# Kernel tuning notes

Measured on AMD Instinct MI355X. Metric: run time of the kernel, lower is better.

## Reference

```python
import jax, jax.numpy as jnp
import numpy as np
from jax import lax

B, N, DIM, H, HD = 4, 8192, 256, 8, 32
INTERNAL = H * HD  # 256
SCALE = HD ** -0.5


def rotate_every_two(x):
    x1 = x[..., ::2]
    x2 = x[..., 1::2]
    return jnp.stack([-x2, x1], axis=-1).reshape(x.shape)


def theta_shift(x, sin, cos):
    # sin/cos: (N, HD) broadcast against (B, H, N, HD)
    return x * cos + rotate_every_two(x) * sin


def setup_inputs() -> dict:
    key = jax.random.key(0)
    ks = jax.random.split(key, 8)
    x = jax.random.normal(ks[0], (B, N, DIM), jnp.float32)
    sin = jax.random.uniform(ks[1], (N, HD), jnp.float32)
    cos = jax.random.uniform(ks[2], (N, HD), jnp.float32)
    W_qkvo = jax.random.normal(ks[3], (4 * INTERNAL, DIM), jnp.float32) * 0.02
    b_qkvo = jnp.zeros((4 * INTERNAL,), jnp.float32)
    W_lepe = jax.random.normal(ks[4], (INTERNAL, 1, 3), jnp.float32) * 0.1  # depthwise conv (O, I/g=1, K)
    b_lepe = jnp.zeros((INTERNAL,), jnp.float32)
    W_proj = jax.random.normal(ks[5], (DIM, INTERNAL), jnp.float32) * 0.02
    b_proj = jnp.zeros((DIM,), jnp.float32)
    return {"x": x, "sin": sin, "cos": cos, "W_qkvo": W_qkvo, "b_qkvo": b_qkvo,
            "W_lepe": W_lepe, "b_lepe": b_lepe, "W_proj": W_proj, "b_proj": b_proj}


def reference(x, sin, cos, W_qkvo, b_qkvo, W_lepe, b_lepe, W_proj, b_proj):
    # qkvo projection and chunk
    qkvo = x @ W_qkvo.T + b_qkvo  # (B, N, 4*INTERNAL)
    q, k, v, o = jnp.split(qkvo, 4, axis=-1)

    # depthwise conv LEPE branch on v: (B, C, N)
    v_t = jnp.transpose(v, (0, 2, 1))
    lepe = lax.conv_general_dilated(
        v_t, W_lepe, window_strides=(1,), padding=[(1, 1)],
        dimension_numbers=("NCH", "OIH", "NCH"), feature_group_count=INTERNAL)
    lepe_out = jnp.transpose(lepe + b_lepe[None, :, None], (0, 2, 1))  # (B, N, INTERNAL)

    # split heads: (B, H, N, HD)
    def heads(t):
        return jnp.transpose(t.reshape(B, N, H, HD), (0, 2, 1, 3))
    qh, kh, vh = heads(q), heads(k), heads(v)

    qh = jax.nn.elu(qh) + 1.0
    kh = jax.nn.elu(kh) + 1.0

    # z: (B, H, N, 1) against per-head k mean
    kmean = kh.mean(axis=2, keepdims=True)  # (B, H, 1, HD)
    z = jnp.einsum("bhnd,bhmd->bhnm", qh, kmean) * SCALE

    qs = theta_shift(qh, sin, cos)
    ks_ = theta_shift(kh, sin, cos)

    s = (SCALE / N) ** 0.5
    kv_state = jnp.einsum("bhnd,bhne->bhde", ks_ * s, vh * s)  # (B, H, HD, HD)
    attn_out = jnp.einsum("bhnd,bhde->bhne", qs, kv_state)     # (B, H, N, HD)

    v_mean = vh.mean(axis=2, keepdims=True)  # (B, H, 1, HD)
    res = attn_out * (1.0 + 1.0 / (z + 1e-6)) - z * v_mean

    res = jnp.transpose(res, (0, 2, 1, 3)).reshape(B, N, INTERNAL)
    res = res + lepe_out
    return (res * o) @ W_proj.T + b_proj
```

## Files before the change

### kernel.cpp

```cpp
#include <hip/hip_runtime.h>
#include <hip/hip_bf16.h>


typedef __bf16 bf16x8 __attribute__((ext_vector_type(8)));
typedef float  f32x4  __attribute__((ext_vector_type(4)));
typedef float  f32x2  __attribute__((ext_vector_type(2)));

#define NSEQ  8192
#define TOK   32768
#define SCALE_F 0.17677669529663687f
#define S2_F    2.1579674718339462e-05f

__device__ __forceinline__ bf16x8 ld8(const __bf16* p) { return *(const bf16x8*)p; }
__device__ __forceinline__ bf16x8 ld8(const float* p) {
  f32x4 a = *(const f32x4*)p;
  f32x4 b = *(const f32x4*)(p + 4);
  bf16x8 r;
  r[0]=(__bf16)a.x; r[1]=(__bf16)a.y; r[2]=(__bf16)a.z; r[3]=(__bf16)a.w;
  r[4]=(__bf16)b.x; r[5]=(__bf16)b.y; r[6]=(__bf16)b.z; r[7]=(__bf16)b.w;
  return r;
}

template<int EPI, typename TA, typename TB, typename TO>
__global__ __launch_bounds__(256)
void gemm_kernel(const TA* __restrict__ A, const TB* __restrict__ Bw,
                 const float* __restrict__ bias,
                 TO* __restrict__ o0, __bf16* __restrict__ o1,
                 __bf16* __restrict__ o2, __bf16* __restrict__ o3)
{
  constexpr int K = 256;
  __shared__ __align__(16) __bf16 As[128*32];
  __shared__ __align__(16) __bf16 Bs[128*32];
  const int tid  = threadIdx.x;
  const int lane = tid & 63;
  const int wid  = tid >> 6;
  const int wm = wid & 1, wn = wid >> 1;
  const long m0 = (long)blockIdx.x * 128;
  const int  n0 = blockIdx.y * 128;

  const TA* ag = A  + (m0 + (tid>>2))*K + (tid&3)*8;
  const TB* bg = Bw + (long)(n0 + (tid>>2))*K + (tid&3)*8;
  __bf16* asw = As + tid*8;
  __bf16* bsw = Bs + tid*8;

  f32x4 acc[4][4] = {};

  for (int k0 = 0; k0 < K; k0 += 32) {
    bf16x8 a0 = ld8(ag + k0);
    bf16x8 a1 = ld8(ag + 64*K + k0);
    bf16x8 b0 = ld8(bg + k0);
    bf16x8 b1 = ld8(bg + 64*K + k0);
    __syncthreads();
    *(bf16x8*)asw          = a0;
    *(bf16x8*)(asw + 2048) = a1;
    *(bf16x8*)bsw          = b0;
    *(bf16x8*)(bsw + 2048) = b1;
    __syncthreads();
    const int row = lane & 15;
    const int k8  = (lane >> 4) * 8;
    bf16x8 af[4], bfr[4];
#pragma unroll
    for (int i=0;i<4;i++) af[i]  = *(const bf16x8*)&As[(wm*64 + i*16 + row)*32 + k8];
#pragma unroll
    for (int j=0;j<4;j++) bfr[j] = *(const bf16x8*)&Bs[(wn*64 + j*16 + row)*32 + k8];
#pragma unroll
    for (int i=0;i<4;i++)
#pragma unroll
      for (int j=0;j<4;j++)
        acc[i][j] = __builtin_amdgcn_mfma_f32_16x16x32_bf16(af[i], bfr[j], acc[i][j], 0,0,0);
  }

#pragma unroll
  for (int i=0;i<4;i++) {
    const long t = m0 + wm*64 + i*16 + (lane>>4)*4;
#pragma unroll
    for (int j=0;j<4;j++) {
      const int cj = n0 + wn*64 + j*16 + (lane&15);
      const float bv = bias[cj];
      if (EPI == 1) {
        const int sec = cj >> 8;
        const int c   = cj & 255;
#pragma unroll
        for (int r=0;r<4;r++) {
          const long tt = t + r;
          float v = acc[i][j][r] + bv;
          if (sec < 2) v = (v > 0.f) ? (v + 1.f) : __expf(v);
          if (sec == 1) {
            const long bh = (tt >> 13)*8 + (c >> 5);
            o1[(bh*8192 + (tt & 8191))*32 + (c & 31)] = (__bf16)v;
          } else {
            __bf16* dst = (sec==0)?(__bf16*)o0:(sec==2)?o2:o3;
            dst[tt*256 + c] = (__bf16)v;
          }
        }
      } else {
#pragma unroll
        for (int r=0;r<4;r++)
          o0[(t+r)*256 + cj] = (TO)(acc[i][j][r] + bv);
      }
    }
  }
}

__global__ __launch_bounds__(256)
void reduce_kernel(const __bf16* __restrict__ kh_t, const __bf16* __restrict__ vv,
                   const float* __restrict__ sing, const float* __restrict__ cosg,
                   float* __restrict__ ksum, float* __restrict__ vsum,
                   float* __restrict__ kvT)
{
  __shared__ __align__(16) float ks_s[128*36];
  __shared__ __align__(16) float v_s[128*36];
  __shared__ float ksum_s[32], vsum_s[32];
  __shared__ float kvacc[1024];
  const int tid = threadIdx.x, lane = tid & 63, wid = tid >> 6;
  const int bh = blockIdx.x;
  const int b = bh >> 3, h = bh & 7;
  const int n0 = blockIdx.y * 512;
  const int seg = tid & 3;
  const int tksl = tid >> 2;

  if (tid < 32) { ksum_s[tid] = 0.f; vsum_s[tid] = 0.f; }
  for (int i = tid; i < 1024; i += 256) kvacc[i] = 0.f;

  float sk[8] = {}, sv[8] = {};
  f32x4 a0={},a1={},a2={},a3={};
  const int db = (lane>>3)*4, eb = (lane&7)*4;

  for (int sub = 0; sub < 4; sub++) {
    const int nbase = n0 + sub*128;
    __syncthreads();
#pragma unroll
    for (int i=0;i<2;i++) {
      const int tok = i*64 + tksl;
      const int n = nbase + tok;
      bf16x8 k8 = *(const bf16x8*)&kh_t[((long)bh*8192 + n)*32 + seg*8];
      bf16x8 w8 = *(const bf16x8*)&vv[((long)b*8192 + n)*256 + h*32 + seg*8];
      f32x4 cA = *(const f32x4*)&cosg[n*32 + seg*8];
      f32x4 cB = *(const f32x4*)&cosg[n*32 + seg*8 + 4];
      f32x4 sA = *(const f32x4*)&sing[n*32 + seg*8];
      f32x4 sB = *(const f32x4*)&sing[n*32 + seg*8 + 4];
      float kf[8], wf[8], cf[8], sf[8], ks[8];
#pragma unroll
      for (int j=0;j<8;j++) { kf[j]=(float)k8[j]; wf[j]=(float)w8[j]; }
      cf[0]=cA.x;cf[1]=cA.y;cf[2]=cA.z;cf[3]=cA.w;cf[4]=cB.x;cf[5]=cB.y;cf[6]=cB.z;cf[7]=cB.w;
      sf[0]=sA.x;sf[1]=sA.y;sf[2]=sA.z;sf[3]=sA.w;sf[4]=sB.x;sf[5]=sB.y;sf[6]=sB.z;sf[7]=sB.w;
#pragma unroll
      for (int j=0;j<8;j+=2) {
        ks[j]   = kf[j]*cf[j]     - kf[j+1]*sf[j];
        ks[j+1] = kf[j+1]*cf[j+1] + kf[j]*sf[j+1];
      }
      f32x4 q0 = {ks[0],ks[1],ks[2],ks[3]}, q1 = {ks[4],ks[5],ks[6],ks[7]};
      *(f32x4*)&ks_s[tok*36 + seg*8]     = q0;
      *(f32x4*)&ks_s[tok*36 + seg*8 + 4] = q1;
      f32x4 p0 = {wf[0],wf[1],wf[2],wf[3]}, p1 = {wf[4],wf[5],wf[6],wf[7]};
      *(f32x4*)&v_s[tok*36 + seg*8]     = p0;
      *(f32x4*)&v_s[tok*36 + seg*8 + 4] = p1;
#pragma unroll
      for (int j=0;j<8;j++) { sk[j] += kf[j]; sv[j] += wf[j]; }
    }
    __syncthreads();
    for (int t2 = 0; t2 < 32; t2++) {
      const int nl = wid*32 + t2;
      f32x4 kk = *(const f32x4*)&ks_s[nl*36 + db];
      f32x4 vp = *(const f32x4*)&v_s[nl*36 + eb];
      a0 += kk.x * vp;  a1 += kk.y * vp;  a2 += kk.z * vp;  a3 += kk.w * vp;
    }
  }

#pragma unroll
  for (int e=0;e<4;e++) {
    atomicAdd(&kvacc[(eb+e)*32 + db+0], a0[e]);
    atomicAdd(&kvacc[(eb+e)*32 + db+1], a1[e]);
    atomicAdd(&kvacc[(eb+e)*32 + db+2], a2[e]);
    atomicAdd(&kvacc[(eb+e)*32 + db+3], a3[e]);
  }
#pragma unroll
  for (int m = 4; m <= 32; m <<= 1) {
#pragma unroll
    for (int j=0;j<8;j++) { sk[j] += __shfl_xor(sk[j], m); sv[j] += __shfl_xor(sv[j], m); }
  }
  if (lane < 4) {
#pragma unroll
    for (int j=0;j<8;j++) {
      atomicAdd(&ksum_s[lane*8 + j], sk[j]);
      atomicAdd(&vsum_s[lane*8 + j], sv[j]);
    }
  }
  __syncthreads();
  float* dst = kvT + (long)bh*1024;
  for (int i = tid; i < 1024; i += 256) atomicAdd(&dst[i], kvacc[i]);
  if (tid < 32) { atomicAdd(&ksum[bh*32+tid], ksum_s[tid]);
                  atomicAdd(&vsum[bh*32+tid], vsum_s[tid]); }
}

__global__ __launch_bounds__(256)
void epi_kernel(const __bf16* __restrict__ qh, const __bf16* __restrict__ vv,
                const __bf16* __restrict__ oo,
                const float* __restrict__ sing, const float* __restrict__ cosg,
                const float* __restrict__ ksum, const float* __restrict__ vsum,
                const float* __restrict__ kvT,
                const float* __restrict__ Wl, const float* __restrict__ bl,
                __bf16* __restrict__ resf)
{
  __shared__ __align__(16) __bf16 qs_s[32*256];
  __shared__ __align__(16) __bf16 kv_s[8*32*32];
  __shared__ __align__(16) __bf16 lep_s[32*256];
  __shared__ float z_s[32*8];
  __shared__ float km_s[256], vm_s[256];
  const int tid = threadIdx.x, lane = tid & 63, wid = tid >> 6;
  const long t0 = (long)blockIdx.x * 32;
  const int b  = (int)(t0 >> 13);
  const int n0 = (int)(t0 & 8191);
  const int bh0 = b * 8;

  for (int i = tid; i < 8192; i += 256)
    kv_s[i] = (__bf16)(kvT[(long)bh0*1024 + i] * S2_F);
  km_s[tid] = ksum[bh0*32 + tid] * (1.f/8192.f);
  vm_s[tid] = vsum[bh0*32 + tid] * (1.f/8192.f);
  __syncthreads();

  for (int i=0;i<16;i++) {
    const int p  = i*256 + tid;
    const int t  = p >> 7;
    const int c2 = p & 127;
    const int h  = c2 >> 4;
    const int d0 = (c2 & 15) * 2;
    const long tg = t0 + t;
    const int n = n0 + t;
    const float q0 = (float)qh[tg*256 + h*32 + d0];
    const float q1 = (float)qh[tg*256 + h*32 + d0 + 1];
    f32x2 cp = *(const f32x2*)&cosg[n*32 + d0];
    f32x2 sp = *(const f32x2*)&sing[n*32 + d0];
    qs_s[t*256 + h*32 + d0]     = (__bf16)(q0*cp.x - q1*sp.x);
    qs_s[t*256 + h*32 + d0 + 1] = (__bf16)(q1*cp.y + q0*sp.y);
    float zp = q0*km_s[h*32+d0] + q1*km_s[h*32+d0+1];
    zp += __shfl_xor(zp, 1);
    zp += __shfl_xor(zp, 2);
    zp += __shfl_xor(zp, 4);
    zp += __shfl_xor(zp, 8);
    if ((lane & 15) == 0) z_s[t*8 + h] = zp * SCALE_F;
  }
  for (int i=0;i<32;i++) {
    const int f = i*256 + tid;
    const int t = f >> 8;
    const int c = f & 255;
    const long tg = t0 + t;
    const int n = n0 + t;
    const float vm1 = (n > 0)      ? (float)vv[(tg-1)*256 + c] : 0.f;
    const float v0  =                (float)vv[tg*256 + c];
    const float vp1 = (n < NSEQ-1) ? (float)vv[(tg+1)*256 + c] : 0.f;
    lep_s[f] = (__bf16)(vm1*Wl[c*3+0] + v0*Wl[c*3+1] + vp1*Wl[c*3+2] + bl[c]);
  }
  __syncthreads();

  const int e  = lane & 15;
  const int d8 = (lane >> 4) * 8;
  for (int hh=0; hh<2; hh++) {
    const int h = wid*2 + hh;
    bf16x8 bfr0 = *(const bf16x8*)&kv_s[h*1024 + e*32 + d8];
    bf16x8 bfr1 = *(const bf16x8*)&kv_s[h*1024 + (16+e)*32 + d8];
    for (int im=0; im<2; im++) {
      bf16x8 afr = *(const bf16x8*)&qs_s[(im*16 + e)*256 + h*32 + d8];
      for (int jn=0; jn<2; jn++) {
        f32x4 acc = {};
        acc = __builtin_amdgcn_mfma_f32_16x16x32_bf16(afr, jn ? bfr1 : bfr0, acc, 0,0,0);
        const int c = h*32 + jn*16 + e;
        const float vmn = vm_s[c];
#pragma unroll
        for (int r=0;r<4;r++) {
          const int t = im*16 + (lane>>4)*4 + r;
          const long tg = t0 + t;
          const float zv = z_s[t*8 + h];
          const float res = acc[r]*(1.f + 1.f/(zv + 1e-6f)) - zv*vmn
                            + (float)lep_s[t*256 + c];
          resf[tg*256 + c] = (__bf16)(res * (float)oo[tg*256 + c]);
        }
      }
    }
  }
}

extern "C" void kernel_launch(void* const* d_in, const int* in_sizes, int n_in,
                              void* d_out, int out_size, void* d_ws, size_t ws_size,
                              hipStream_t stream)
{
  const float* x    = (const float*)d_in[0];
  const float* sing = (const float*)d_in[1];
  const float* cosg = (const float*)d_in[2];
  const float* Wq   = (const float*)d_in[3];
  const float* bq   = (const float*)d_in[4];
  const float* Wl   = (const float*)d_in[5];
  const float* bl   = (const float*)d_in[6];
  const float* Wp   = (const float*)d_in[7];
  const float* bp   = (const float*)d_in[8];
  float* out = (float*)d_out;

  char* ws = (char*)d_ws;
  float*  ksum = (float*)(ws);
  float*  vsum = (float*)(ws + 4096);
  float*  kvT  = (float*)(ws + 8192);
  const size_t T0 = 256 * 1024;
  const size_t SZ = (size_t)TOK * 256 * sizeof(__bf16);
  __bf16* kh_t = (__bf16*)(ws + T0);
  __bf16* vv   = (__bf16*)(ws + T0 + SZ);
  __bf16* oo   = (__bf16*)(ws + T0 + 2*SZ);
  __bf16* qh   = (__bf16*)(ws + T0 + 3*SZ);
  __bf16* resf = kh_t;

  hipMemsetAsync(ws, 0, 8192 + 32*1024*4, stream);

  gemm_kernel<1,float,float,__bf16><<<dim3(256, 8), 256, 0, stream>>>(x, Wq, bq, qh, kh_t, vv, oo);
  reduce_kernel<<<dim3(32, 16), 256, 0, stream>>>(kh_t, vv, sing, cosg, ksum, vsum, kvT);
  epi_kernel<<<1024, 256, 0, stream>>>(qh, vv, oo, sing, cosg, ksum, vsum, kvT, Wl, bl, resf);
  gemm_kernel<2,__bf16,float,float><<<dim3(256, 2), 256, 0, stream>>>(resf, Wp, bp, out, nullptr, nullptr, nullptr);
}
```

Measured before the change: 225.2 us.

## Pre-convert GEMM inputs to bf16 and load tiles via global_load_lds

Adds conversion kernels that turn x and both weight matrices into bf16 buffers in workspace, so both GEMMs read only bf16. Tile staging then uses direct global-to-LDS loads instead of loading through registers and storing to shared memory. The aim is to shrink register traffic and conversion work inside the GEMM loop. In exchange it adds three launches and an extra full pass over x (read fp32, write bf16). The epilogue output buffer is moved to reuse the converted-x buffer.

Measured after the change: 213.3 us. -5.3%, faster.

```diff
diff --git a/kernel.cpp b/kernel.cpp
--- a/kernel.cpp
+++ b/kernel.cpp
@@ -11,8 +11,13 @@
 #define SCALE_F 0.17677669529663687f
 #define S2_F    2.1579674718339462e-05f
 
-__device__ __forceinline__ bf16x8 ld8(const __bf16* p) { return *(const bf16x8*)p; }
-__device__ __forceinline__ bf16x8 ld8(const float* p) {
+__device__ __forceinline__ void gld16(void* lds, const void* g) {
+  __builtin_amdgcn_global_load_lds((const __attribute__((address_space(1))) void*)g,
+                                   (__attribute__((address_space(3))) void*)lds,
+                                   16, 0, 0);
+}
+
+__device__ __forceinline__ bf16x8 cvt8(const float* p) {
   f32x4 a = *(const f32x4*)p;
   f32x4 b = *(const f32x4*)(p + 4);
   bf16x8 r;
@@ -21,9 +26,17 @@
   return r;
 }
 
-template<int EPI, typename TA, typename TB, typename TO>
 __global__ __launch_bounds__(256)
-void gemm_kernel(const TA* __restrict__ A, const TB* __restrict__ Bw,
+void cvt_kernel(const float* __restrict__ src, __bf16* __restrict__ dst, int n8)
+{
+  const int i = blockIdx.x*256 + threadIdx.x;
+  if (i >= n8) return;
+  *(bf16x8*)(dst + (long)i*8) = cvt8(src + (long)i*8);
+}
+
+template<int EPI, typename TO>
+__global__ __launch_bounds__(256)
+void gemm_kernel(const __bf16* __restrict__ A, const __bf16* __restrict__ Bw,
                  const float* __restrict__ bias,
                  TO* __restrict__ o0, __bf16* __restrict__ o1,
                  __bf16* __restrict__ o2, __bf16* __restrict__ o3)
@@ -38,23 +51,19 @@
   const long m0 = (long)blockIdx.x * 128;
   const int  n0 = blockIdx.y * 128;
 
-  const TA* ag = A  + (m0 + (tid>>2))*K + (tid&3)*8;
-  const TB* bg = Bw + (long)(n0 + (tid>>2))*K + (tid&3)*8;
+  const __bf16* ag = A  + (m0 + (tid>>2))*K + (tid&3)*8;
+  const __bf16* bg = Bw + (long)(n0 + (tid>>2))*K + (tid&3)*8;
   __bf16* asw = As + tid*8;
   __bf16* bsw = Bs + tid*8;
 
   f32x4 acc[4][4] = {};
 
   for (int k0 = 0; k0 < K; k0 += 32) {
-    bf16x8 a0 = ld8(ag + k0);
-    bf16x8 a1 = ld8(ag + 64*K + k0);
-    bf16x8 b0 = ld8(bg + k0);
-    bf16x8 b1 = ld8(bg + 64*K + k0);
     __syncthreads();
-    *(bf16x8*)asw          = a0;
-    *(bf16x8*)(asw + 2048) = a1;
-    *(bf16x8*)bsw          = b0;
-    *(bf16x8*)(bsw + 2048) = b1;
+    gld16(asw,        ag + k0);
+    gld16(asw + 2048, ag + 64*K + k0);
+    gld16(bsw,        bg + k0);
+    gld16(bsw + 2048, bg + 64*K + k0);
     __syncthreads();
     const int row = lane & 15;
     const int k8  = (lane >> 4) * 8;
@@ -305,12 +314,19 @@
   __bf16* vv   = (__bf16*)(ws + T0 + SZ);
   __bf16* oo   = (__bf16*)(ws + T0 + 2*SZ);
   __bf16* qh   = (__bf16*)(ws + T0 + 3*SZ);
-  __bf16* resf = kh_t;
+  __bf16* xbf  = (__bf16*)(ws + T0 + 4*SZ);
+  __bf16* Wqb  = (__bf16*)(ws + T0 + 5*SZ);
+  __bf16* Wpb  = (__bf16*)(ws + T0 + 5*SZ + 512*1024);
+  __bf16* resf = xbf;
 
   hipMemsetAsync(ws, 0, 8192 + 32*1024*4, stream);
 
-  gemm_kernel<1,float,float,__bf16><<<dim3(256, 8), 256, 0, stream>>>(x, Wq, bq, qh, kh_t, vv, oo);
+  cvt_kernel<<<4096, 256, 0, stream>>>(x,  xbf, TOK*256/8);
+  cvt_kernel<<<128,  256, 0, stream>>>(Wq, Wqb, 1024*256/8);
+  cvt_kernel<<<32,   256, 0, stream>>>(Wp, Wpb, 256*256/8);
+
+  gemm_kernel<1,__bf16><<<dim3(256, 8), 256, 0, stream>>>(xbf, Wqb, bq, qh, kh_t, vv, oo);
   reduce_kernel<<<dim3(32, 16), 256, 0, stream>>>(kh_t, vv, sing, cosg, ksum, vsum, kvT);
   epi_kernel<<<1024, 256, 0, stream>>>(qh, vv, oo, sing, cosg, ksum, vsum, kvT, Wl, bl, resf);
-  gemm_kernel<2,__bf16,float,float><<<dim3(256, 2), 256, 0, stream>>>(resf, Wp, bp, out, nullptr, nullptr, nullptr);
-}
+  gemm_kernel<2,float><<<dim3(256, 2), 256, 0, stream>>>(resf, Wpb, bp, out, nullptr, nullptr, nullptr);
+}
```
